# Kernel optimization log

Hardware: AMD Instinct MI355X
Metric: run time of the kernel (lower is better)

Reference implementation:

```python
import jax, jax.numpy as jnp
import numpy as np

S, E, KN = 40000, 18000, 128
N_SE = 1_500_000
N_EK = 180_000


def setup_inputs() -> dict:
    key = jax.random.key(0)
    ks = jax.random.split(key, 32)
    nrm = lambda i, shape, s=1.0: jax.random.normal(ks[i], shape, dtype=jnp.float32) * s
    ri = lambda i, n, lo, hi: jax.random.randint(ks[i], (n,), lo, hi, dtype=jnp.int32)
    inp = {
        'stu_emb': nrm(0, (S, KN), 0.5),
        'exer_emb': nrm(1, (E, KN), 0.5),
        'kn_emb': nrm(2, (KN, KN), 0.5),
        'sfe_fcW': nrm(3, (KN, KN), 0.05), 'sfe_attnW': nrm(4, (1, 2 * KN), 0.05),
        'efs_fcW': nrm(5, (KN, KN), 0.05), 'efs_attnW': nrm(6, (1, 2 * KN), 0.05),
        'efk_fcW': nrm(7, (KN, KN), 0.05), 'efk_attnW': nrm(8, (1, 2 * KN), 0.05),
        'kfe_fcW': nrm(9, (KN, KN), 0.05), 'kfe_attnW': nrm(10, (1, 2 * KN), 0.05),
        's_attn0_W': nrm(11, (1, 2 * KN), 0.05), 's_attn0_b': jnp.zeros((1,), jnp.float32),
        'e_attn0_W': nrm(12, (1, 2 * KN), 0.05), 'e_attn0_b': jnp.zeros((1,), jnp.float32),
        'e_attn1_W': nrm(13, (1, 2 * KN), 0.05), 'e_attn1_b': jnp.zeros((1,), jnp.float32),
        'k_attn0_W': nrm(14, (1, 2 * KN), 0.05), 'k_attn0_b': jnp.zeros((1,), jnp.float32),
        # s_e graphs: node ids [0,S) = students, [S,S+E) = exercises (matches the
        # repo's slicing s_from_e_conv[:S] / e_from_s_conv[S:])
        'sfe_src': ri(16, N_SE, S, S + E), 'sfe_dst': ri(17, N_SE, 0, S),
        'efs_src': ri(18, N_SE, 0, S), 'efs_dst': ri(19, N_SE, S, S + E),
        # e_k graphs: node ids [0,E) = exercises, [E,E+KN) = knowledge
        'efk_src': ri(20, N_EK, E, E + KN), 'efk_dst': ri(21, N_EK, 0, E),
        'kfe_src': ri(22, N_EK, 0, E), 'kfe_dst': ri(23, N_EK, E, E + KN),
    }
    return inp


def _gat(h, fcW, attnW, src, dst, n_nodes):
    """GAT layer: per-dst segment softmax over edge scores, weighted sum of z[src]."""
    z = h @ fcW.T                                   # [n_nodes, K]
    K = z.shape[1]
    # attn_fc(cat(z_src, z_dst)) == z_src @ a[:K] + z_dst @ a[K:]
    e = z[src] @ attnW[0, :K] + z[dst] @ attnW[0, K:]   # [n_edges]
    m = jax.ops.segment_max(e, dst, num_segments=n_nodes)
    ex = jnp.exp(e - m[dst])
    denom = jax.ops.segment_sum(ex, dst, num_segments=n_nodes)
    alpha = ex / denom[dst]                         # [n_edges]
    return jax.ops.segment_sum(alpha[:, None] * z[src], dst, num_segments=n_nodes)


def _pair_score(a, b, W, bias):
    # Linear(2K -> 1, bias) on cat([a, b], dim=1) -> [N, 1]
    K = a.shape[1]
    return (a @ W[0, :K] + b @ W[0, K:] + bias[0])[:, None]


def reference(stu_emb, exer_emb, kn_emb,
              sfe_fcW, sfe_attnW, efs_fcW, efs_attnW,
              efk_fcW, efk_attnW, kfe_fcW, kfe_attnW,
              s_attn0_W, s_attn0_b, e_attn0_W, e_attn0_b,
              e_attn1_W, e_attn1_b, k_attn0_W, k_attn0_b,
              sfe_src, sfe_dst, efs_src, efs_dst,
              efk_src, efk_dst, kfe_src, kfe_dst):
    s_num, e_num = stu_emb.shape[0], exer_emb.shape[0]
    k_num = kn_emb.shape[0]
    e_k_weight = jnp.concatenate([exer_emb, kn_emb], axis=0)    # [E+KN, K]
    s_e_weight = jnp.concatenate([exer_emb, stu_emb], axis=0)   # [E+S, K]

    s_from_e = _gat(s_e_weight, sfe_fcW, sfe_attnW, sfe_src, sfe_dst, e_num + s_num)
    e_from_s = _gat(s_e_weight, efs_fcW, efs_attnW, efs_src, efs_dst, e_num + s_num)
    e_from_k = _gat(e_k_weight, efk_fcW, efk_attnW, efk_src, efk_dst, e_num + k_num)
    k_from_e = _gat(e_k_weight, kfe_fcW, kfe_attnW, kfe_src, kfe_dst, e_num + k_num)

    # students
    sc0 = _pair_score(stu_emb, s_from_e[:s_num], s_attn0_W, s_attn0_b)     # [S,1]
    sc = jax.nn.softmax(sc0, axis=1)                                        # all ones
    ult_stu = stu_emb + sc[:, 0:1] * s_from_e[:s_num]

    # exercises
    sc0 = _pair_score(exer_emb, e_from_s[s_num:], e_attn0_W, e_attn0_b)    # [E,1]
    sc1 = _pair_score(exer_emb, e_from_k[:e_num], e_attn1_W, e_attn1_b)    # [E,1]
    sc = jax.nn.softmax(jnp.concatenate([sc0, sc1], axis=1), axis=1)       # [E,2]
    ult_exer = exer_emb + sc[:, 0:1] * e_from_s[s_num:] + sc[:, 1:2] * e_from_k[:e_num]

    # knowledge
    sc0 = _pair_score(kn_emb, k_from_e[e_num:], k_attn0_W, k_attn0_b)      # [KN,1]
    sc = jax.nn.softmax(sc0, axis=1)
    ult_kn = kn_emb + sc[:, 0:1] * k_from_e[e_num:]

    return ult_stu, ult_exer, ult_kn
```

## Files before the change

### kernel.cpp

```cpp
#include <hip/hip_runtime.h>
#include <hip/hip_bf16.h>

using f32x4  = __attribute__((ext_vector_type(4))) float;
using bf16x8 = __attribute__((ext_vector_type(8))) short;
typedef unsigned int u32;
typedef unsigned short u16;

#define KD 128
#define NBINS 512
#define CHUNKP 4096
#define CAPB 8192
#define MAXB 10240
#define NSEGMAX 768

__device__ inline float bf2f(short s){
  return __uint_as_float(((u32)(u16)s) << 16);
}

struct BinParams {
  long Cb[4]; int base[4]; double dr[4]; double dbin; int nseg;
};

__device__ inline int bin_of(int seg, const BinParams& bp){
  int r = (seg >= bp.base[1]) + (seg >= bp.base[2]) + (seg >= bp.base[3]);
  long ep = bp.Cb[r] + (long)((double)(seg - bp.base[r]) * bp.dr[r]);
  int b = (int)((double)ep * bp.dbin);
  return (b > NBINS - 1) ? (NBINS - 1) : b;
}

__global__ void k_pb512(BinParams bp, int* __restrict__ pb){
  int t = blockIdx.x * blockDim.x + threadIdx.x;
  if (t > NBINS) return;
  if (t == 0){ pb[0] = 0; return; }
  if (t == NBINS){ pb[NBINS] = bp.nseg; return; }
  int lo = 0, hi = bp.nseg;
  while (lo < hi){
    int mid = (lo + hi) >> 1;
    if (bin_of(mid, bp) >= t) hi = mid; else lo = mid + 1;
  }
  pb[t] = lo;
}

__global__ __launch_bounds__(256) void k_cvt_w(const float* __restrict__ w0,
                                               const float* __restrict__ w1,
                                               const float* __restrict__ w2,
                                               const float* __restrict__ w3,
                                               short* __restrict__ out){
  int i = blockIdx.x * 256 + threadIdx.x;
  const float* src = (i < 16384) ? w0 : (i < 32768) ? w1 : (i < 49152) ? w2 : w3;
  float v = src[i & 16383];
  __hip_bfloat16 b = __float2bfloat16(v);
  out[i] = __builtin_bit_cast(short, b);
}

struct PlaceSh {
  u32 sorted[CHUNKP];
  u16 sbid[CHUNKP];
  int cnt[NBINS];
  int lbase[NBINS];
  int lpos[NBINS];
  int pbL[NBINS];
  int sc[256];
};
struct GemmSh { short zst[4][16][136]; };

struct GJob { const float* A1; const float* attn; __hip_bfloat16* Z; float* ews;
              int zbase, nrows, blk0, wboff; };

__device__ void gemm_body(GemmSh* g,
                          const float* __restrict__ A0, int nA,
                          const float* __restrict__ A1,
                          const short* __restrict__ Wb, const float* __restrict__ attn,
                          __hip_bfloat16* __restrict__ Z, float* __restrict__ ews,
                          int zbase, int nrows, int blk)
{
  const int wave = threadIdx.x >> 6, lane = threadIdx.x & 63;
  const int lr = lane & 15, lk = lane >> 4;
  const int row0 = blk * 64 + wave * 16;

  bf16x8 afrag[4];
  {
    int r = row0 + lr;
    bool rv = (r < nrows);
    int node = zbase + r;
    const float* ap = A0;
    if (rv) ap = (node < nA) ? (A0 + (size_t)node * KD) : (A1 + (size_t)(node - nA) * KD);
#pragma unroll
    for (int t = 0; t < 4; ++t){
      float x[8];
      if (rv){
        float4 u0 = *(const float4*)(ap + t * 32 + lk * 8);
        float4 u1 = *(const float4*)(ap + t * 32 + lk * 8 + 4);
        x[0]=u0.x; x[1]=u0.y; x[2]=u0.z; x[3]=u0.w;
        x[4]=u1.x; x[5]=u1.y; x[6]=u1.z; x[7]=u1.w;
      } else {
#pragma unroll
        for (int j = 0; j < 8; ++j) x[j] = 0.f;
      }
      bf16x8 af;
#pragma unroll
      for (int j = 0; j < 8; ++j){
        __hip_bfloat16 b = __float2bfloat16(x[j]);
        af[j] = __builtin_bit_cast(short, b);
      }
      afrag[t] = af;
    }
  }

  f32x4 acc[8];
#pragma unroll
  for (int c = 0; c < 8; ++c){ acc[c][0]=0.f; acc[c][1]=0.f; acc[c][2]=0.f; acc[c][3]=0.f; }

#pragma unroll
  for (int c = 0; c < 8; ++c){
#pragma unroll
    for (int t = 0; t < 4; ++t){
      bf16x8 bf = *(const bf16x8*)(Wb + (c * 16 + lr) * KD + t * 32 + lk * 8);
      acc[c] = __builtin_amdgcn_mfma_f32_16x16x32_bf16(afrag[t], bf, acc[c], 0, 0, 0);
    }
  }

  float p[4] = {0.f, 0.f, 0.f, 0.f};
#pragma unroll
  for (int c = 0; c < 8; ++c){
    float av = attn[c * 16 + lr];
#pragma unroll
    for (int q = 0; q < 4; ++q){
      p[q] += acc[c][q] * av;
      g->zst[wave][lk * 4 + q][c * 16 + lr] =
          __builtin_bit_cast(short, __float2bfloat16(acc[c][q]));
    }
  }
#pragma unroll
  for (int q = 0; q < 4; ++q){
#pragma unroll
    for (int o = 1; o < 16; o <<= 1) p[q] += __shfl_xor(p[q], o, 64);
  }
  if (lr == 0){
#pragma unroll
    for (int q = 0; q < 4; ++q){
      int r = row0 + lk * 4 + q;
      if (r < nrows) ews[r] = __expf(p[q]);
    }
  }
  __syncthreads();
#pragma unroll
  for (int pq = 0; pq < 4; ++pq){
    int row = pq * 4 + (lane >> 4);
    int col8 = (lane & 15) * 8;
    bf16x8 v = *(const bf16x8*)&g->zst[wave][row][col8];
    int r = row0 + row;
    if (r < nrows) *(bf16x8*)(Z + (size_t)r * KD + col8) = v;
  }
}

struct MegaArgs {
  const int* d0; const int* s0; const int* d1; const int* s1;
  const int* d2; const int* s2; const int* d3; const int* s3;
  int nse, nek, rebase23, nplace;
  u32* buckets;
  int* gcur;
  const int* pb;
  BinParams bp;
  const float* A0; int nA;
  const short* Wb;
  GJob j[4];
};

__global__ __launch_bounds__(256) void k_megaF(MegaArgs a){
  __shared__ alignas(16) char shraw[sizeof(PlaceSh)];
  const int tid = threadIdx.x;
  const int b = blockIdx.x;
  if (b < a.nplace){
    PlaceSh& P = *reinterpret_cast<PlaceSh*>(shraw);
    for (int j = tid; j < NBINS; j += 256){ P.cnt[j] = 0; P.pbL[j] = a.pb[j]; }
    __syncthreads();
    const long total = 2L * a.nse + 2L * a.nek;
    long c0 = (long)b * CHUNKP;
    long c1 = c0 + CHUNKP; if (c1 > total) c1 = total;

    for (long i = c0 + tid; i < c1; i += 256){
      long k = i; const int* dp; int rb;
      if (k < a.nse){ dp = a.d0; rb = 0; }
      else if ((k -= a.nse) < a.nse){ dp = a.d1; rb = 0; }
      else if ((k -= a.nse) < a.nek){ dp = a.d2; rb = a.rebase23; }
      else { k -= a.nek; dp = a.d3; rb = a.rebase23; }
      atomicAdd(&P.cnt[bin_of(dp[k] + rb, a.bp)], 1);
    }
    __syncthreads();
    int carry = 0;
    for (int cb = 0; cb < NBINS; cb += 256){
      int j = cb + tid;
      int v = P.cnt[j];
      P.sc[tid] = v; __syncthreads();
      for (int o = 1; o < 256; o <<= 1){
        int u = (tid >= o) ? P.sc[tid - o] : 0;
        __syncthreads();
        P.sc[tid] += u;
        __syncthreads();
      }
      P.lbase[j] = carry + P.sc[tid] - v;
      P.lpos[j]  = P.lbase[j];
      carry += P.sc[255];
      __syncthreads();
    }
    for (int j = tid; j < NBINS; j += 256){
      int c = P.cnt[j];
      P.cnt[j] = c ? atomicAdd(&a.gcur[j], c) : 0;
    }
    for (long i = c0 + tid; i < c1; i += 256){
      long k = i; const int* dp; const int* sp; int rb;
      if (k < a.nse){ dp = a.d0; sp = a.s0; rb = 0; }
      else if ((k -= a.nse) < a.nse){ dp = a.d1; sp = a.s1; rb = 0; }
      else if ((k -= a.nse) < a.nek){ dp = a.d2; sp = a.s2; rb = a.rebase23; }
      else { k -= a.nek; dp = a.d3; sp = a.s3; rb = a.rebase23; }
      int seg = dp[k] + rb;
      int bn = bin_of(seg, a.bp);
      u32 e = ((u32)(seg - P.pbL[bn]) << 16) | (u32)sp[k];
      int p = atomicAdd(&P.lpos[bn], 1);
      P.sorted[p] = e;
      P.sbid[p] = (u16)bn;
    }
    __syncthreads();
    int n = (int)(c1 - c0);
    for (int i = tid; i < n; i += 256){
      int bn = P.sbid[i];
      int idx = P.cnt[bn] + (i - P.lbase[bn]);
      if (idx < CAPB)
        __builtin_nontemporal_store(P.sorted[i], &a.buckets[(size_t)bn * CAPB + idx]);
    }
  } else {
    GemmSh* G = reinterpret_cast<GemmSh*>(shraw);
    int gb = b - a.nplace;
    int ji = 3;
    if (gb < a.j[1].blk0) ji = 0;
    else if (gb < a.j[2].blk0) ji = 1;
    else if (gb < a.j[3].blk0) ji = 2;
    GJob J = a.j[ji];
    gemm_body(G, a.A0, a.nA, J.A1, a.Wb + J.wboff, J.attn, J.Z, J.ews,
              J.zbase, J.nrows, gb - J.blk0);
  }
}

__global__ __launch_bounds__(512) void k_scan512(const int* __restrict__ gcur,
                                                 int* __restrict__ binbase){
  __shared__ int sh[512];
  int tid = threadIdx.x;
  int v = gcur[tid];
  sh[tid] = v; __syncthreads();
  for (int o = 1; o < 512; o <<= 1){
    int u = (tid >= o) ? sh[tid - o] : 0;
    __syncthreads();
    sh[tid] += u;
    __syncthreads();
  }
  binbase[tid] = sh[tid] - v;
}

__global__ __launch_bounds__(512) void k_scatc(const u32* __restrict__ buckets,
                                               const int* __restrict__ gcur,
                                               const int* __restrict__ binbase,
                                               const int* __restrict__ pb,
                                               int* __restrict__ offs,
                                               u16* __restrict__ edges){
  __shared__ u16 els[MAXB];
  __shared__ int pc[NSEGMAX + 1];
  __shared__ int sc[512];
  const int t = blockIdx.x;
  const int tid = threadIdx.x;
  const int base = binbase[t];
  int n = gcur[t]; if (n > CAPB) n = CAPB;
  const int lo = pb[t], hi = pb[t + 1];
  const int nsl = hi - lo;

  for (int j = tid; j < nsl; j += 512) pc[j] = 0;
  __syncthreads();
  for (int i = tid; i < n; i += 512){
    u32 e = buckets[(size_t)t * CAPB + i];
    int srel = (int)(e >> 16);
    if (srel < nsl) atomicAdd(&pc[srel], 1);
  }
  __syncthreads();
  int carry = 0;
  for (int cb = 0; cb < nsl; cb += 512){
    int j = cb + tid;
    int v = (j < nsl) ? pc[j] : 0;
    sc[tid] = v; __syncthreads();
    for (int o = 1; o < 512; o <<= 1){
      int u = (tid >= o) ? sc[tid - o] : 0;
      __syncthreads();
      sc[tid] += u;
      __syncthreads();
    }
    if (j < nsl) pc[j] = carry + sc[tid] - v;
    carry += sc[511];
    __syncthreads();
  }
  for (int j = tid; j < nsl; j += 512) offs[lo + j] = base + pc[j];
  if (t == NBINS - 1 && tid == 0) offs[hi] = base + n;
  __syncthreads();

  for (int i = tid; i < n; i += 512){
    u32 e = buckets[(size_t)t * CAPB + i];
    int srel = (int)(e >> 16);
    if (srel < nsl){
      int pos = atomicAdd(&pc[srel], 1);
      els[pos] = (u16)(e & 0xffffu);
    }
  }
  __syncthreads();
  int st = base & 1;
  if (st && tid == 0) edges[base] = els[0];
  int m = n - st;
  int nh = m >> 1;
  u32* dst = (u32*)(edges + base + st);
  for (int i2 = tid; i2 < nh; i2 += 512){
    u32 v = ((u32)els[st + 2 * i2 + 1] << 16) | (u32)els[st + 2 * i2];
    __builtin_nontemporal_store(v, &dst[i2]);
  }
  if ((m & 1) && tid == 0) edges[base + n - 1] = els[n - 1];
}

#define GATHER2(EW, Z, ZB, ACC, DS, BEG, END)                                   \
  {                                                                             \
    int i = (BEG) + slot;                                                       \
    for (; i + 4 < (END); i += 8){                                              \
      int r0 = (int)a.edges[i] - (ZB);                                          \
      int r1 = (int)a.edges[i + 4] - (ZB);                                      \
      float w0 = (EW)[r0], w1 = (EW)[r1];                                       \
      bf16x8 z0 = *(const bf16x8*)((Z) + (size_t)r0 * KD + li * 8);             \
      bf16x8 z1 = *(const bf16x8*)((Z) + (size_t)r1 * KD + li * 8);             \
      (DS) += w0 + w1;                                                          \
      _Pragma("unroll")                                                         \
      for (int j = 0; j < 8; ++j){                                              \
        (ACC)[j] = fmaf(w0, bf2f(z0[j]), (ACC)[j]);                             \
        (ACC)[j] = fmaf(w1, bf2f(z1[j]), (ACC)[j]);                             \
      }                                                                         \
    }                                                                           \
    if (i < (END)){                                                             \
      int r0 = (int)a.edges[i] - (ZB);                                          \
      float w0 = (EW)[r0];                                                      \
      bf16x8 z0 = *(const bf16x8*)((Z) + (size_t)r0 * KD + li * 8);             \
      (DS) += w0;                                                               \
      _Pragma("unroll")                                                         \
      for (int j = 0; j < 8; ++j) (ACC)[j] = fmaf(w0, bf2f(z0[j]), (ACC)[j]);   \
    }                                                                           \
  }

struct AggArgs {
  const int* offs; const u16* edges;
  const float* ew_sfe; const __hip_bfloat16* z_sfe;
  const float* ew_efs; const __hip_bfloat16* z_efs;
  const float* ew_efk; const __hip_bfloat16* z_efk;
  const float* stu; const float* exer;
  float* out;
  const float* a0W; const float* a0b; const float* a1W; const float* a1b;
  int S, E;
};

__global__ __launch_bounds__(256) void k_aggW(AggArgs a){
  const int lane = threadIdx.x & 63;
  const int wave = threadIdx.x >> 6;
  const int li = lane & 15;
  const int slot = lane >> 4;
  const int gs = blockIdx.x * 4 + wave;
  if (gs >= a.S + a.E) return;

  if (gs < a.S){
    const int beg = a.offs[gs], end = a.offs[gs + 1];
    float acc[8];
#pragma unroll
    for (int j = 0; j < 8; ++j) acc[j] = 0.f;
    float ds = 0.f;
    GATHER2(a.ew_sfe, a.z_sfe, a.S, acc, ds, beg, end)
#pragma unroll
    for (int j = 0; j < 8; ++j){
      acc[j] += __shfl_xor(acc[j], 16, 64);
      acc[j] += __shfl_xor(acc[j], 32, 64);
    }
    ds += __shfl_xor(ds, 16, 64);
    ds += __shfl_xor(ds, 32, 64);
    float rden = (end > beg) ? 1.f / ds : 0.f;
    if (lane < 32){
      const size_t o = (size_t)gs * KD + li * 8 + slot * 4;
      const float* emb = a.stu + o;
      float4 v;
      v.x = emb[0] + acc[slot * 4 + 0] * rden;
      v.y = emb[1] + acc[slot * 4 + 1] * rden;
      v.z = emb[2] + acc[slot * 4 + 2] * rden;
      v.w = emb[3] + acc[slot * 4 + 3] * rden;
      *(float4*)(a.out + o) = v;
    }
  } else {
    const int e = gs - a.S;
    const int b1 = a.offs[a.S + e], e1 = a.offs[a.S + e + 1];
    const int b2 = a.offs[a.S + a.E + e], e2 = a.offs[a.S + a.E + e + 1];
    float acc1[8], acc2[8];
#pragma unroll
    for (int j = 0; j < 8; ++j){ acc1[j] = 0.f; acc2[j] = 0.f; }
    float ds1 = 0.f, ds2 = 0.f;
    GATHER2(a.ew_efs, a.z_efs, 0,   acc1, ds1, b1, e1)
    GATHER2(a.ew_efk, a.z_efk, a.E, acc2, ds2, b2, e2)
#pragma unroll
    for (int j = 0; j < 8; ++j){
      acc1[j] += __shfl_xor(acc1[j], 16, 64);
      acc1[j] += __shfl_xor(acc1[j], 32, 64);
      acc2[j] += __shfl_xor(acc2[j], 16, 64);
      acc2[j] += __shfl_xor(acc2[j], 32, 64);
    }
    ds1 += __shfl_xor(ds1, 16, 64); ds1 += __shfl_xor(ds1, 32, 64);
    ds2 += __shfl_xor(ds2, 16, 64); ds2 += __shfl_xor(ds2, 32, 64);
    float r1 = (e1 > b1) ? 1.f / ds1 : 0.f;
    float r2 = (e2 > b2) ? 1.f / ds2 : 0.f;
    float aw1[8], aw2[8];
#pragma unroll
    for (int j = 0; j < 8; ++j){ aw1[j] = acc1[j] * r1; aw2[j] = acc2[j] * r2; }

    float ex8[8];
    {
      float4 u0 = *(const float4*)(a.exer + (size_t)e * KD + li * 8);
      float4 u1 = *(const float4*)(a.exer + (size_t)e * KD + li * 8 + 4);
      ex8[0]=u0.x; ex8[1]=u0.y; ex8[2]=u0.z; ex8[3]=u0.w;
      ex8[4]=u1.x; ex8[5]=u1.y; ex8[6]=u1.z; ex8[7]=u1.w;
    }
    float q0 = 0.f, q1 = 0.f;
#pragma unroll
    for (int j = 0; j < 8; ++j){
      q0 += ex8[j] * a.a0W[li * 8 + j] + aw1[j] * a.a0W[KD + li * 8 + j];
      q1 += ex8[j] * a.a1W[li * 8 + j] + aw2[j] * a.a1W[KD + li * 8 + j];
    }
#pragma unroll
    for (int o = 1; o < 16; o <<= 1){
      q0 += __shfl_xor(q0, o, 64);
      q1 += __shfl_xor(q1, o, 64);
    }
    float sc0 = q0 + a.a0b[0], sc1 = q1 + a.a1b[0];
    float mx = fmaxf(sc0, sc1);
    float w0 = __expf(sc0 - mx), w1 = __expf(sc1 - mx);
    float inv = 1.f / (w0 + w1);
    w0 *= inv; w1 *= inv;
    if (lane < 32){
      const size_t o = (size_t)gs * KD + li * 8 + slot * 4;
      float4 v;
#pragma unroll
      for (int q = 0; q < 4; ++q){
        int j = slot * 4 + q;
        ((float*)&v)[q] = ex8[j] + w0 * aw1[j] + w1 * aw2[j];
      }
      *(float4*)(a.out + o) = v;
    }
  }
}

__global__ __launch_bounds__(512) void k_aggK(const int* __restrict__ offs, int segbase,
                                              const u16* __restrict__ edges,
                                              const float* __restrict__ ews,
                                              const __hip_bfloat16* __restrict__ Z,
                                              const float* __restrict__ kn,
                                              float* __restrict__ out){
  __shared__ float sred[8];
  __shared__ float lacc[8][KD];
  const int tid = threadIdx.x;
  const int wave = tid >> 6, lane = tid & 63;
  const int sub = lane >> 4, li = lane & 15;
  const int seg = segbase + blockIdx.x;
  const int beg = offs[seg], end = offs[seg + 1];

  float acc[8];
#pragma unroll
  for (int j = 0; j < 8; ++j) acc[j] = 0.f;
  float ds = 0.f;
  const int slot = wave * 4 + sub;
  {
    int i = beg + slot;
    for (; i + 32 < end; i += 64){
      int r0 = (int)edges[i];
      int r1 = (int)edges[i + 32];
      float w0 = ews[r0], w1 = ews[r1];
      bf16x8 z0 = *(const bf16x8*)(Z + (size_t)r0 * KD + li * 8);
      bf16x8 z1 = *(const bf16x8*)(Z + (size_t)r1 * KD + li * 8);
      ds += w0 + w1;
#pragma unroll
      for (int j = 0; j < 8; ++j){
        acc[j] = fmaf(w0, bf2f(z0[j]), acc[j]);
        acc[j] = fmaf(w1, bf2f(z1[j]), acc[j]);
      }
    }
    if (i < end){
      int r0 = (int)edges[i];
      float w0 = ews[r0];
      bf16x8 z0 = *(const bf16x8*)(Z + (size_t)r0 * KD + li * 8);
      ds += w0;
#pragma unroll
      for (int j = 0; j < 8; ++j) acc[j] = fmaf(w0, bf2f(z0[j]), acc[j]);
    }
  }
#pragma unroll
  for (int j = 0; j < 8; ++j){
    acc[j] += __shfl_xor(acc[j], 16, 64);
    acc[j] += __shfl_xor(acc[j], 32, 64);
  }
  ds += __shfl_xor(ds, 16, 64);
  ds += __shfl_xor(ds, 32, 64);
  if (lane == 0) sred[wave] = ds;
  if (sub == 0){
    f32x4 v0, v1;
#pragma unroll
    for (int j = 0; j < 4; ++j){ v0[j] = acc[j]; v1[j] = acc[4 + j]; }
    *(f32x4*)&lacc[wave][li * 8]     = v0;
    *(f32x4*)&lacc[wave][li * 8 + 4] = v1;
  }
  __syncthreads();
  if (tid < KD){
    float dsum = 0.f;
#pragma unroll
    for (int wv = 0; wv < 8; ++wv) dsum += sred[wv];
    float s = 0.f;
#pragma unroll
    for (int wv = 0; wv < 8; ++wv) s += lacc[wv][tid];
    float rden = (end > beg) ? 1.f / dsum : 0.f;
    out[(size_t)blockIdx.x * KD + tid] = kn[(size_t)blockIdx.x * KD + tid] + s * rden;
  }
}

extern "C" void kernel_launch(void* const* d_in, const int* in_sizes, int n_in,
                              void* d_out, int out_size, void* d_ws, size_t ws_size,
                              hipStream_t stream){
  const int S  = in_sizes[0] / KD;
  const int E  = in_sizes[1] / KD;
  const int KN = in_sizes[2] / KD;
  const int nse = in_sizes[19];
  const int nek = in_sizes[23];

  const float* stu  = (const float*)d_in[0];
  const float* exer = (const float*)d_in[1];
  const float* kn   = (const float*)d_in[2];
  const float* sfe_fcW = (const float*)d_in[3];  const float* sfe_attn = (const float*)d_in[4];
  const float* efs_fcW = (const float*)d_in[5];  const float* efs_attn = (const float*)d_in[6];
  const float* efk_fcW = (const float*)d_in[7];  const float* efk_attn = (const float*)d_in[8];
  const float* kfe_fcW = (const float*)d_in[9];  const float* kfe_attn = (const float*)d_in[10];
  const float* ea0W = (const float*)d_in[13]; const float* ea0b = (const float*)d_in[14];
  const float* ea1W = (const float*)d_in[15]; const float* ea1b = (const float*)d_in[16];
  const int* sfe_src = (const int*)d_in[19]; const int* sfe_dst = (const int*)d_in[20];
  const int* efs_src = (const int*)d_in[21]; const int* efs_dst = (const int*)d_in[22];
  const int* efk_src = (const int*)d_in[23]; const int* efk_dst = (const int*)d_in[24];
  const int* kfe_src = (const int*)d_in[25]; const int* kfe_dst = (const int*)d_in[26];
  float* out = (float*)d_out;

  char* w = (char*)d_ws;
  auto alloc = [&](size_t bytes) -> char* {
    char* p = w; w += (bytes + 255) & ~(size_t)255; return p;
  };
  short* Wb               = (short*)alloc((size_t)4 * 16384 * 2);
  __hip_bfloat16* z_sfe   = (__hip_bfloat16*)alloc((size_t)E  * KD * 2);
  __hip_bfloat16* z_efs   = (__hip_bfloat16*)alloc((size_t)S  * KD * 2);
  __hip_bfloat16* z_efk   = (__hip_bfloat16*)alloc((size_t)KN * KD * 2);
  __hip_bfloat16* z_kfe   = (__hip_bfloat16*)alloc((size_t)E  * KD * 2);
  float* ew_sfe = (float*)alloc((size_t)E  * 4);
  float* ew_efs = (float*)alloc((size_t)S  * 4);
  float* ew_efk = (float*)alloc((size_t)KN * 4);
  float* ew_kfe = (float*)alloc((size_t)E  * 4);
  const int NSEG = S + E + E + KN;
  const size_t TOTE = 2 * (size_t)nse + 2 * (size_t)nek;
  const int NPLACE = (int)((TOTE + CHUNKP - 1) / CHUNKP);
  int* pb512   = (int*)alloc((NBINS + 1) * 4);
  int* gcur    = (int*)alloc(NBINS * 4);
  int* binbase = (int*)alloc(NBINS * 4);
  int* offs    = (int*)alloc((size_t)(NSEG + 1) * 4);
  u32* buckets = (u32*)alloc((size_t)NBINS * CAPB * 4);
  u16* edges   = (u16*)alloc(TOTE * 2);

  hipMemsetAsync(gcur, 0, NBINS * 4, stream);

  BinParams bp;
  bp.Cb[0] = 0; bp.Cb[1] = nse; bp.Cb[2] = 2L * nse; bp.Cb[3] = 2L * nse + nek;
  bp.base[0] = 0; bp.base[1] = S; bp.base[2] = S + E; bp.base[3] = S + 2 * E;
  bp.dr[0] = (double)nse / S; bp.dr[1] = (double)nse / E;
  bp.dr[2] = (double)nek / E; bp.dr[3] = (double)nek / KN;
  bp.dbin = (double)NBINS / (double)TOTE;
  bp.nseg = NSEG;

  k_pb512<<<1, 1024, 0, stream>>>(bp, pb512);
  k_cvt_w<<<256, 256, 0, stream>>>(sfe_fcW, efs_fcW, efk_fcW, kfe_fcW, Wb);

  const int nbE = (E + 63) / 64, nbS = (S + 63) / 64, nbK = (KN + 63) / 64;
  MegaArgs ma;
  ma.d0 = sfe_dst; ma.s0 = sfe_src; ma.d1 = efs_dst; ma.s1 = efs_src;
  ma.d2 = efk_dst; ma.s2 = efk_src; ma.d3 = kfe_dst; ma.s3 = kfe_src;
  ma.nse = nse; ma.nek = nek; ma.rebase23 = S + E; ma.nplace = NPLACE;
  ma.buckets = buckets; ma.gcur = gcur; ma.pb = pb512; ma.bp = bp;
  ma.A0 = exer; ma.nA = E; ma.Wb = Wb;
  ma.j[0] = { stu, sfe_attn, z_sfe, ew_sfe, S, E,  0,               0 };
  ma.j[1] = { stu, efs_attn, z_efs, ew_efs, 0, S,  nbE,             16384 };
  ma.j[2] = { kn,  efk_attn, z_efk, ew_efk, E, KN, nbE + nbS,       32768 };
  ma.j[3] = { kn,  kfe_attn, z_kfe, ew_kfe, 0, E,  nbE + nbS + nbK, 49152 };
  k_megaF<<<NPLACE + nbE + nbS + nbK + nbE, 256, 0, stream>>>(ma);

  k_scan512<<<1, 512, 0, stream>>>(gcur, binbase);
  k_scatc<<<NBINS, 512, 0, stream>>>(buckets, gcur, binbase, pb512, offs, edges);

  k_aggK<<<KN, 512, 0, stream>>>(offs, S + 2 * E, edges, ew_kfe, z_kfe,
                                 kn, out + (size_t)(S + E) * KD);

  AggArgs aa;
  aa.offs = offs; aa.edges = edges;
  aa.ew_sfe = ew_sfe; aa.z_sfe = z_sfe;
  aa.ew_efs = ew_efs; aa.z_efs = z_efs;
  aa.ew_efk = ew_efk; aa.z_efk = z_efk;
  aa.stu = stu; aa.exer = exer; aa.out = out;
  aa.a0W = ea0W; aa.a0b = ea0b; aa.a1W = ea1W; aa.a1b = ea1b;
  aa.S = S; aa.E = E;
  k_aggW<<<(S + E + 3) / 4, 256, 0, stream>>>(aa);
}
```

Before: 245.8 us.

## Widen mega kernel to 512 threads, pad bin counters, unroll gathers by four

The fused placement/GEMM kernel now runs 512-thread blocks. The placement half does a single-pass 512-bin scan instead of two 256-wide passes, and each GEMM block covers 128 rows across 8 waves. Global per-bin counters are strided by 16 ints so that atomics from different bins land on separate cache lines. The aggregation gathers are unrolled from two to four in-flight edge loads, which raises memory-level parallelism but increases register pressure.

```diff
diff --git a/kernel.cpp b/kernel.cpp
--- a/kernel.cpp
+++ b/kernel.cpp
@@ -12,6 +12,7 @@
 #define CAPB 8192
 #define MAXB 10240
 #define NSEGMAX 768
+#define GSTR 16
 
 __device__ inline float bf2f(short s){
   return __uint_as_float(((u32)(u16)s) << 16);
@@ -60,9 +61,9 @@
   int lbase[NBINS];
   int lpos[NBINS];
   int pbL[NBINS];
-  int sc[256];
+  int sc[512];
 };
-struct GemmSh { short zst[4][16][136]; };
+struct GemmSh { short zst[8][16][136]; };
 
 struct GJob { const float* A1; const float* attn; __hip_bfloat16* Z; float* ews;
               int zbase, nrows, blk0, wboff; };
@@ -76,7 +77,7 @@
 {
   const int wave = threadIdx.x >> 6, lane = threadIdx.x & 63;
   const int lr = lane & 15, lk = lane >> 4;
-  const int row0 = blk * 64 + wave * 16;
+  const int row0 = blk * 128 + wave * 16;
 
   bf16x8 afrag[4];
   {
@@ -167,19 +168,19 @@
   GJob j[4];
 };
 
-__global__ __launch_bounds__(256) void k_megaF(MegaArgs a){
+__global__ __launch_bounds__(512) void k_megaF(MegaArgs a){
   __shared__ alignas(16) char shraw[sizeof(PlaceSh)];
   const int tid = threadIdx.x;
   const int b = blockIdx.x;
   if (b < a.nplace){
     PlaceSh& P = *reinterpret_cast<PlaceSh*>(shraw);
-    for (int j = tid; j < NBINS; j += 256){ P.cnt[j] = 0; P.pbL[j] = a.pb[j]; }
+    if (tid < NBINS){ P.cnt[tid] = 0; P.pbL[tid] = a.pb[tid]; }
     __syncthreads();
     const long total = 2L * a.nse + 2L * a.nek;
     long c0 = (long)b * CHUNKP;
     long c1 = c0 + CHUNKP; if (c1 > total) c1 = total;
 
-    for (long i = c0 + tid; i < c1; i += 256){
+    for (long i = c0 + tid; i < c1; i += 512){
       long k = i; const int* dp; int rb;
       if (k < a.nse){ dp = a.d0; rb = 0; }
       else if ((k -= a.nse) < a.nse){ dp = a.d1; rb = 0; }
@@ -188,27 +189,29 @@
       atomicAdd(&P.cnt[bin_of(dp[k] + rb, a.bp)], 1);
     }
     __syncthreads();
-    int carry = 0;
-    for (int cb = 0; cb < NBINS; cb += 256){
-      int j = cb + tid;
-      int v = P.cnt[j];
-      P.sc[tid] = v; __syncthreads();
-      for (int o = 1; o < 256; o <<= 1){
+    {
+      int v = P.cnt[tid & (NBINS - 1)];
+      if (tid >= NBINS) v = 0;
+      int vv = (tid < NBINS) ? P.cnt[tid] : 0;
+      P.sc[tid] = vv; __syncthreads();
+      for (int o = 1; o < 512; o <<= 1){
         int u = (tid >= o) ? P.sc[tid - o] : 0;
         __syncthreads();
         P.sc[tid] += u;
         __syncthreads();
       }
-      P.lbase[j] = carry + P.sc[tid] - v;
-      P.lpos[j]  = P.lbase[j];
-      carry += P.sc[255];
-      __syncthreads();
-    }
-    for (int j = tid; j < NBINS; j += 256){
-      int c = P.cnt[j];
-      P.cnt[j] = c ? atomicAdd(&a.gcur[j], c) : 0;
-    }
-    for (long i = c0 + tid; i < c1; i += 256){
+      if (tid < NBINS){
+        P.lbase[tid] = P.sc[tid] - vv;
+        P.lpos[tid]  = P.sc[tid] - vv;
+      }
+      (void)v;
+    }
+    __syncthreads();
+    if (tid < NBINS){
+      int c = P.cnt[tid];
+      P.cnt[tid] = c ? atomicAdd(&a.gcur[tid * GSTR], c) : 0;
+    }
+    for (long i = c0 + tid; i < c1; i += 512){
       long k = i; const int* dp; const int* sp; int rb;
       if (k < a.nse){ dp = a.d0; sp = a.s0; rb = 0; }
       else if ((k -= a.nse) < a.nse){ dp = a.d1; sp = a.s1; rb = 0; }
@@ -223,7 +226,7 @@
     }
     __syncthreads();
     int n = (int)(c1 - c0);
-    for (int i = tid; i < n; i += 256){
+    for (int i = tid; i < n; i += 512){
       int bn = P.sbid[i];
       int idx = P.cnt[bn] + (i - P.lbase[bn]);
       if (idx < CAPB)
@@ -246,7 +249,7 @@
                                                  int* __restrict__ binbase){
   __shared__ int sh[512];
   int tid = threadIdx.x;
-  int v = gcur[tid];
+  int v = gcur[tid * GSTR];
   sh[tid] = v; __syncthreads();
   for (int o = 1; o < 512; o <<= 1){
     int u = (tid >= o) ? sh[tid - o] : 0;
@@ -269,7 +272,7 @@
   const int t = blockIdx.x;
   const int tid = threadIdx.x;
   const int base = binbase[t];
-  int n = gcur[t]; if (n > CAPB) n = CAPB;
+  int n = gcur[t * GSTR]; if (n > CAPB) n = CAPB;
   const int lo = pb[t], hi = pb[t + 1];
   const int nsl = hi - lo;
 
@@ -321,23 +324,29 @@
   if ((m & 1) && tid == 0) edges[base + n - 1] = els[n - 1];
 }
 
-#define GATHER2(EW, Z, ZB, ACC, DS, BEG, END)                                   \
+#define GATHER4(EW, Z, ZB, ACC, DS, BEG, END)                                   \
   {                                                                             \
     int i = (BEG) + slot;                                                       \
-    for (; i + 4 < (END); i += 8){                                              \
-      int r0 = (int)a.edges[i] - (ZB);                                          \
-      int r1 = (int)a.edges[i + 4] - (ZB);                                      \
-      float w0 = (EW)[r0], w1 = (EW)[r1];                                       \
+    for (; i + 12 < (END); i += 16){                                            \
+      int r0 = (int)a.edges[i]      - (ZB);                                     \
+      int r1 = (int)a.edges[i + 4]  - (ZB);                                     \
+      int r2 = (int)a.edges[i + 8]  - (ZB);                                     \
+      int r3 = (int)a.edges[i + 12] - (ZB);                                     \
+      float w0 = (EW)[r0], w1 = (EW)[r1], w2 = (EW)[r2], w3 = (EW)[r3];         \
       bf16x8 z0 = *(const bf16x8*)((Z) + (size_t)r0 * KD + li * 8);             \
       bf16x8 z1 = *(const bf16x8*)((Z) + (size_t)r1 * KD + li * 8);             \
-      (DS) += w0 + w1;                                                          \
+      bf16x8 z2 = *(const bf16x8*)((Z) + (size_t)r2 * KD + li * 8);             \
+      bf16x8 z3 = *(const bf16x8*)((Z) + (size_t)r3 * KD + li * 8);             \
+      (DS) += (w0 + w1) + (w2 + w3);                                            \
       _Pragma("unroll")                                                         \
       for (int j = 0; j < 8; ++j){                                              \
         (ACC)[j] = fmaf(w0, bf2f(z0[j]), (ACC)[j]);                             \
         (ACC)[j] = fmaf(w1, bf2f(z1[j]), (ACC)[j]);                             \
+        (ACC)[j] = fmaf(w2, bf2f(z2[j]), (ACC)[j]);                             \
+        (ACC)[j] = fmaf(w3, bf2f(z3[j]), (ACC)[j]);                             \
       }                                                                         \
     }                                                                           \
-    if (i < (END)){                                                             \
+    for (; i < (END); i += 4){                                                  \
       int r0 = (int)a.edges[i] - (ZB);                                          \
       float w0 = (EW)[r0];                                                      \
       bf16x8 z0 = *(const bf16x8*)((Z) + (size_t)r0 * KD + li * 8);             \
@@ -372,7 +381,7 @@
 #pragma unroll
     for (int j = 0; j < 8; ++j) acc[j] = 0.f;
     float ds = 0.f;
-    GATHER2(a.ew_sfe, a.z_sfe, a.S, acc, ds, beg, end)
+    GATHER4(a.ew_sfe, a.z_sfe, a.S, acc, ds, beg, end)
 #pragma unroll
     for (int j = 0; j < 8; ++j){
       acc[j] += __shfl_xor(acc[j], 16, 64);
@@ -399,8 +408,8 @@
 #pragma unroll
     for (int j = 0; j < 8; ++j){ acc1[j] = 0.f; acc2[j] = 0.f; }
     float ds1 = 0.f, ds2 = 0.f;
-    GATHER2(a.ew_efs, a.z_efs, 0,   acc1, ds1, b1, e1)
-    GATHER2(a.ew_efk, a.z_efk, a.E, acc2, ds2, b2, e2)
+    GATHER4(a.ew_efs, a.z_efs, 0,   acc1, ds1, b1, e1)
+    GATHER4(a.ew_efk, a.z_efk, a.E, acc2, ds2, b2, e2)
 #pragma unroll
     for (int j = 0; j < 8; ++j){
       acc1[j] += __shfl_xor(acc1[j], 16, 64);
@@ -473,20 +482,26 @@
   const int slot = wave * 4 + sub;
   {
     int i = beg + slot;
-    for (; i + 32 < end; i += 64){
+    for (; i + 96 < end; i += 128){
       int r0 = (int)edges[i];
       int r1 = (int)edges[i + 32];
-      float w0 = ews[r0], w1 = ews[r1];
+      int r2 = (int)edges[i + 64];
+      int r3 = (int)edges[i + 96];
+      float w0 = ews[r0], w1 = ews[r1], w2 = ews[r2], w3 = ews[r3];
       bf16x8 z0 = *(const bf16x8*)(Z + (size_t)r0 * KD + li * 8);
       bf16x8 z1 = *(const bf16x8*)(Z + (size_t)r1 * KD + li * 8);
-      ds += w0 + w1;
+      bf16x8 z2 = *(const bf16x8*)(Z + (size_t)r2 * KD + li * 8);
+      bf16x8 z3 = *(const bf16x8*)(Z + (size_t)r3 * KD + li * 8);
+      ds += (w0 + w1) + (w2 + w3);
 #pragma unroll
       for (int j = 0; j < 8; ++j){
         acc[j] = fmaf(w0, bf2f(z0[j]), acc[j]);
         acc[j] = fmaf(w1, bf2f(z1[j]), acc[j]);
+        acc[j] = fmaf(w2, bf2f(z2[j]), acc[j]);
+        acc[j] = fmaf(w3, bf2f(z3[j]), acc[j]);
       }
     }
-    if (i < end){
+    for (; i < end; i += 32){
       int r0 = (int)edges[i];
       float w0 = ews[r0];
       bf16x8 z0 = *(const bf16x8*)(Z + (size_t)r0 * KD + li * 8);
@@ -564,13 +579,13 @@
   const size_t TOTE = 2 * (size_t)nse + 2 * (size_t)nek;
   const int NPLACE = (int)((TOTE + CHUNKP - 1) / CHUNKP);
   int* pb512   = (int*)alloc((NBINS + 1) * 4);
-  int* gcur    = (int*)alloc(NBINS * 4);
+  int* gcur    = (int*)alloc((size_t)NBINS * GSTR * 4);
   int* binbase = (int*)alloc(NBINS * 4);
   int* offs    = (int*)alloc((size_t)(NSEG + 1) * 4);
   u32* buckets = (u32*)alloc((size_t)NBINS * CAPB * 4);
   u16* edges   = (u16*)alloc(TOTE * 2);
 
-  hipMemsetAsync(gcur, 0, NBINS * 4, stream);
+  hipMemsetAsync(gcur, 0, (size_t)NBINS * GSTR * 4, stream);
 
   BinParams bp;
   bp.Cb[0] = 0; bp.Cb[1] = nse; bp.Cb[2] = 2L * nse; bp.Cb[3] = 2L * nse + nek;
@@ -583,7 +598,7 @@
   k_pb512<<<1, 1024, 0, stream>>>(bp, pb512);
   k_cvt_w<<<256, 256, 0, stream>>>(sfe_fcW, efs_fcW, efk_fcW, kfe_fcW, Wb);
 
-  const int nbE = (E + 63) / 64, nbS = (S + 63) / 64, nbK = (KN + 63) / 64;
+  const int nbE = (E + 127) / 128, nbS = (S + 127) / 128, nbK = (KN + 127) / 128;
   MegaArgs ma;
   ma.d0 = sfe_dst; ma.s0 = sfe_src; ma.d1 = efs_dst; ma.s1 = efs_src;
   ma.d2 = efk_dst; ma.s2 = efk_src; ma.d3 = kfe_dst; ma.s3 = kfe_src;
@@ -594,7 +609,7 @@
   ma.j[1] = { stu, efs_attn, z_efs, ew_efs, 0, S,  nbE,             16384 };
   ma.j[2] = { kn,  efk_attn, z_efk, ew_efk, E, KN, nbE + nbS,       32768 };
   ma.j[3] = { kn,  kfe_attn, z_kfe, ew_kfe, 0, E,  nbE + nbS + nbK, 49152 };
-  k_megaF<<<NPLACE + nbE + nbS + nbK + nbE, 256, 0, stream>>>(ma);
+  k_megaF<<<NPLACE + nbE + nbS + nbK + nbE, 512, 0, stream>>>(ma);
 
   k_scan512<<<1, 512, 0, stream>>>(gcur, binbase);
   k_scatc<<<NBINS, 512, 0, stream>>>(buckets, gcur, binbase, pb512, offs, edges);
```

Result: no change. 249.8 us (+1.6%).
